# Kernel optimization log

Measured on AMD Instinct MI355X. Metric: run time of the kernel, lower is better.

Reference implementation:

```python
import jax, jax.numpy as jnp
import numpy as np

NUM_HEADS = 6


def setup_inputs() -> dict:
    key = jax.random.key(0)
    k1, k2, k3 = jax.random.split(key, 3)
    b_, n, c = 512, 256, 192
    nw = 64
    x = jax.random.normal(k1, (b_, n, c), dtype=jnp.float32)
    mask = jnp.zeros((nw, n, n), dtype=jnp.float32)  # 0 / -inf additive window mask
    W_qkv = jax.random.normal(k2, (3 * c, c), dtype=jnp.float32) * 0.02
    W_proj = jax.random.normal(k3, (c, c), dtype=jnp.float32) * 0.02
    b_proj = jnp.zeros((c,), dtype=jnp.float32)
    return {"x": x, "mask": mask, "W_qkv": W_qkv, "W_proj": W_proj, "b_proj": b_proj}


def reference(x, mask, W_qkv, W_proj, b_proj):
    b_, n, c = x.shape
    h = NUM_HEADS
    d = c // h
    scale = d ** (-0.5)
    # qkv projection (no bias): (b_, n, 3, h, d) -> (3, b_, h, n, d)
    qkv = (x @ W_qkv.T).reshape(b_, n, 3, h, d).transpose(2, 0, 3, 1, 4)
    q, k, v = qkv[0], qkv[1], qkv[2]
    q = q * scale
    attn = jnp.einsum('bhid,bhjd->bhij', q, k)  # (b_, h, n, n)
    nw = mask.shape[0]
    # add per-window mask bias: view as (B, nw, h, n, n) + (1, nw, 1, n, n)
    attn = attn.reshape(b_ // nw, nw, h, n, n) + mask[None, :, None, :, :]
    attn = attn.reshape(b_, h, n, n)
    attn = jax.nn.softmax(attn, axis=-1)
    out = jnp.einsum('bhij,bhjd->bhid', attn, v)  # (b_, h, n, d)
    out = out.transpose(0, 2, 1, 3).reshape(b_, n, c)
    return out @ W_proj.T + b_proj
```

## Files before the change

kernel.cpp:

```cpp
#include <hip/hip_runtime.h>
#include <hip/hip_bf16.h>
#include <stdint.h>

typedef short bf16x8 __attribute__((ext_vector_type(8)));
typedef float f32x4 __attribute__((ext_vector_type(4)));

#define B_   512
#define N_   256
#define C_   192
#define H_   6
#define D_   32
#define NW_  64

__device__ __forceinline__ uint16_t f2bf(float f) {
    uint32_t u = __builtin_bit_cast(uint32_t, f);
    u += 0x7FFFu + ((u >> 16) & 1u);
    return (uint16_t)(u >> 16);
}

__device__ __forceinline__ uint32_t pk_bf16(float a, float b) {
    float2 t; t.x = a; t.y = b;
    __hip_bfloat162 h = __float22bfloat162_rn(t);
    uint32_t u;
    __builtin_memcpy(&u, &h, 4);
    return u;
}

__device__ __forceinline__ bf16x8 ld_bf8(const uint16_t* p) {
    uint4 u = *reinterpret_cast<const uint4*>(p);
    return __builtin_bit_cast(bf16x8, u);
}

__global__ void prep_kernel(const float* __restrict__ mask,
                            const float* __restrict__ wqkv,
                            const float* __restrict__ wproj,
                            uint16_t* __restrict__ sel,
                            uint16_t* __restrict__ wqkv_bf,
                            uint16_t* __restrict__ wproj_bf,
                            unsigned* __restrict__ flag) {
    const int64_t NSEL = (int64_t)NW_ * N_ * N_;
    const int64_t NWQ  = 3 * C_ * C_;
    const int64_t NWP  = (int64_t)C_ * C_;
    int64_t i = (int64_t)blockIdx.x * blockDim.x + threadIdx.x;
    int64_t stride = (int64_t)gridDim.x * blockDim.x;
    bool nz = false;
    for (; i < NSEL + NWQ + NWP; i += stride) {
        if (i < NSEL) {
            float m = mask[i];
            nz |= (m != 0.0f);
            sel[i] = (m == 0.0f) ? 0xFFFFu : 0u;
        } else if (i < NSEL + NWQ) {
            int64_t j = i - NSEL;
            wqkv_bf[j] = f2bf(wqkv[j]);
        } else {
            int64_t j = i - NSEL - NWQ;
            wproj_bf[j] = f2bf(wproj[j]);
        }
    }
    if (flag && __any(nz) && ((threadIdx.x & 63) == 0))
        atomicOr(flag, 1u);
}

#define SA 200
#define SB 72
__global__ __launch_bounds__(512, 4)
void qkv_kernel(const float* __restrict__ x, const uint16_t* __restrict__ wq,
                uint16_t* __restrict__ qbuf, uint16_t* __restrict__ kbuf,
                uint16_t* __restrict__ vtbuf) {
    __shared__ __align__(16) uint16_t Alds[128 * SA];
    __shared__ __align__(16) uint16_t Blds[192 * SB];
    const int tid  = threadIdx.x;
    const int lane = tid & 63;
    const int wv   = tid >> 6;
    const int wrow = wv >> 2;
    const int wcol = wv & 3;
    const int quad = lane >> 4;
    const int l15  = lane & 15;
    const int m0   = blockIdx.x * 128;

#pragma unroll
    for (int p = 0; p < 12; p++) {
        int f = p * 512 + tid;
        int row = f / 48, c4 = f % 48;
        const float4 v = *reinterpret_cast<const float4*>(
            x + (int64_t)(m0 + row) * 192 + c4 * 4);
        uint2 d;
        d.x = pk_bf16(v.x, v.y);
        d.y = pk_bf16(v.z, v.w);
        *reinterpret_cast<uint2*>(&Alds[row * SA + c4 * 4]) = d;
    }

    const float scale = 0.17677669529663687f * 1.4426950408889634f;

    for (int cb = 0; cb < 3; cb++) {
        f32x4 acc[4][3];
#pragma unroll
        for (int i = 0; i < 4; i++)
#pragma unroll
            for (int j = 0; j < 3; j++) acc[i][j] = (f32x4)0.f;

        for (int k0 = 0; k0 < 192; k0 += 64) {
            uint4 wreg[3];
#pragma unroll
            for (int p = 0; p < 3; p++) {
                int u = p * 512 + tid;
                wreg[p] = *reinterpret_cast<const uint4*>(
                    wq + (int64_t)(cb * 192 + (u >> 3)) * 192 + k0 + (u & 7) * 8);
            }
            __syncthreads();
#pragma unroll
            for (int p = 0; p < 3; p++) {
                int u = p * 512 + tid;
                *reinterpret_cast<uint4*>(&Blds[(u >> 3) * SB + (u & 7) * 8]) = wreg[p];
            }
            __syncthreads();
#pragma unroll
            for (int ks = 0; ks < 2; ks++) {
                bf16x8 xf[4], wf[3];
#pragma unroll
                for (int i = 0; i < 4; i++)
                    xf[i] = *reinterpret_cast<const bf16x8*>(
                        &Alds[(wrow * 64 + i * 16 + l15) * SA + k0 + ks * 32 + quad * 8]);
#pragma unroll
                for (int j = 0; j < 3; j++)
                    wf[j] = *reinterpret_cast<const bf16x8*>(
                        &Blds[(wcol * 48 + j * 16 + l15) * SB + ks * 32 + quad * 8]);
                __builtin_amdgcn_s_setprio(1);
                if (cb < 2) {
#pragma unroll
                    for (int i = 0; i < 4; i++)
#pragma unroll
                        for (int j = 0; j < 3; j++)
                            acc[i][j] = __builtin_amdgcn_mfma_f32_16x16x32_bf16(
                                wf[j], xf[i], acc[i][j], 0, 0, 0);
                } else {
#pragma unroll
                    for (int i = 0; i < 4; i++)
#pragma unroll
                        for (int j = 0; j < 3; j++)
                            acc[i][j] = __builtin_amdgcn_mfma_f32_16x16x32_bf16(
                                xf[i], wf[j], acc[i][j], 0, 0, 0);
                }
                __builtin_amdgcn_s_setprio(0);
            }
        }

        if (cb < 2) {
            uint16_t* dst = (cb == 0) ? qbuf : kbuf;
            const float sc = (cb == 0) ? scale : 1.0f;
#pragma unroll
            for (int i = 0; i < 4; i++) {
                int m = m0 + wrow * 64 + i * 16 + l15;
                int b = m >> 8, pos = m & 255;
#pragma unroll
                for (int j = 0; j < 3; j++) {
                    int cbase = wcol * 48 + j * 16 + quad * 4;
                    int h = cbase >> 5, d0 = cbase & 31;
                    int64_t bh = (int64_t)b * H_ + h;
                    uint2 s;
                    s.x = pk_bf16(acc[i][j][0] * sc, acc[i][j][1] * sc);
                    s.y = pk_bf16(acc[i][j][2] * sc, acc[i][j][3] * sc);
                    *reinterpret_cast<uint2*>(&dst[(bh * N_ + pos) * D_ + d0]) = s;
                }
            }
        } else {
#pragma unroll
            for (int i = 0; i < 4; i++) {
                int m = m0 + wrow * 64 + i * 16 + quad * 4;
                int b = m >> 8, pos0 = m & 255;
#pragma unroll
                for (int j = 0; j < 3; j++) {
                    int c = wcol * 48 + j * 16 + l15;
                    int h = c >> 5, d = c & 31;
                    int64_t bh = (int64_t)b * H_ + h;
                    uint2 s;
                    s.x = pk_bf16(acc[i][j][0], acc[i][j][1]);
                    s.y = pk_bf16(acc[i][j][2], acc[i][j][3]);
                    *reinterpret_cast<uint2*>(&vtbuf[(bh * D_ + d) * N_ + pos0]) = s;
                }
            }
        }
    }
}

__global__ __launch_bounds__(256, 3)
void attn_kernel(const uint16_t* __restrict__ qbuf, const uint16_t* __restrict__ kbuf,
                 const uint16_t* __restrict__ vtbuf, const uint16_t* __restrict__ sel,
                 const unsigned* __restrict__ flag,
                 uint16_t* __restrict__ aout) {
    __shared__ __align__(16) uint16_t Plds[4 * 2 * 32 * 40];
    const int bi = blockIdx.x;
    const int h  = bi % 6;
    const int r_ = bi / 6;
    const int ih = r_ & 1;
    const int g  = (r_ >> 1) & 7;
    const int w  = r_ >> 4;
    const int b  = g * 64 + w;
    const int tid  = threadIdx.x;
    const int lane = tid & 63;
    const int wv   = tid >> 6;
    const int quad = lane >> 4;
    const int l15  = lane & 15;
    const int i0   = ih * 128 + wv * 32;
    const bool hasmask = flag ? (*flag != 0u) : true;
    const int64_t bh = (int64_t)b * H_ + h;
    const uint16_t* qB = qbuf  + bh * N_ * D_;
    const uint16_t* kB = kbuf  + bh * N_ * D_;
    const uint16_t* vB = vtbuf + bh * D_ * N_;
    const uint16_t* sB = sel   + (int64_t)w * N_ * N_;
    uint16_t* Pw = &Plds[wv * 2 * 32 * 40];

    bf16x8 qf[2];
#pragma unroll
    for (int it = 0; it < 2; it++)
        qf[it] = ld_bf8(&qB[(i0 + it * 16 + l15) * D_ + quad * 8]);

    f32x4 oacc[2][2];
    f32x4 lacc[2];
#pragma unroll
    for (int mt = 0; mt < 2; mt++) {
        oacc[mt][0] = (f32x4)0.f; oacc[mt][1] = (f32x4)0.f; lacc[mt] = (f32x4)0.f;
    }
    bf16x8 ones;
#pragma unroll
    for (int e = 0; e < 8; e++) ones[e] = (short)0x3F80;

    bf16x8 kf[4];
#pragma unroll
    for (int jt = 0; jt < 4; jt++)
        kf[jt] = ld_bf8(&kB[(jt * 16 + l15) * D_ + quad * 8]);
    bf16x8 vf[2][2];
#pragma unroll
    for (int hf = 0; hf < 2; hf++)
#pragma unroll
        for (int nt = 0; nt < 2; nt++)
            vf[hf][nt] = ld_bf8(&vB[(nt * 16 + l15) * N_ + hf * 32 + quad * 8]);

    for (int jc = 0; jc < 4; jc++) {
        const int j0 = jc * 64;

        bf16x8 kfn[4], vfn[2][2];
        if (jc < 3) {
#pragma unroll
            for (int jt = 0; jt < 4; jt++)
                kfn[jt] = ld_bf8(&kB[(j0 + 64 + jt * 16 + l15) * D_ + quad * 8]);
#pragma unroll
            for (int hf = 0; hf < 2; hf++)
#pragma unroll
                for (int nt = 0; nt < 2; nt++)
                    vfn[hf][nt] = ld_bf8(&vB[(nt * 16 + l15) * N_ + j0 + 64 + hf * 32 + quad * 8]);
        }

        uint4 sv[2][2];
        if (hasmask) {
#pragma unroll
            for (int hf = 0; hf < 2; hf++)
#pragma unroll
                for (int mt = 0; mt < 2; mt++)
                    sv[hf][mt] = *reinterpret_cast<const uint4*>(
                        &sB[(int64_t)(i0 + mt * 16 + l15) * N_ + j0 + hf * 32 + quad * 8]);
        } else {
#pragma unroll
            for (int hf = 0; hf < 2; hf++)
#pragma unroll
                for (int mt = 0; mt < 2; mt++)
                    sv[hf][mt] = make_uint4(~0u, ~0u, ~0u, ~0u);
        }

#pragma unroll
        for (int hf = 0; hf < 2; hf++) {
            f32x4 sacc[2][2];
#pragma unroll
            for (int jt2 = 0; jt2 < 2; jt2++)
#pragma unroll
                for (int it = 0; it < 2; it++) sacc[jt2][it] = (f32x4)0.f;
            __builtin_amdgcn_s_setprio(1);
#pragma unroll
            for (int jt2 = 0; jt2 < 2; jt2++)
#pragma unroll
                for (int it = 0; it < 2; it++)
                    sacc[jt2][it] = __builtin_amdgcn_mfma_f32_16x16x32_bf16(
                        kf[hf * 2 + jt2], qf[it], sacc[jt2][it], 0, 0, 0);
            __builtin_amdgcn_s_setprio(0);

            uint16_t* Ph = Pw + hf * (32 * 40);
#pragma unroll
            for (int it = 0; it < 2; it++)
#pragma unroll
                for (int jt2 = 0; jt2 < 2; jt2++) {
                    f32x4 s = sacc[jt2][it];
                    uint2 d;
                    d.x = pk_bf16(__builtin_amdgcn_exp2f(s[0]),
                                  __builtin_amdgcn_exp2f(s[1]));
                    d.y = pk_bf16(__builtin_amdgcn_exp2f(s[2]),
                                  __builtin_amdgcn_exp2f(s[3]));
                    *reinterpret_cast<uint2*>(
                        &Ph[(it * 16 + l15) * 40 + jt2 * 16 + quad * 4]) = d;
                }

#pragma unroll
            for (int mt = 0; mt < 2; mt++) {
                uint4 p = *reinterpret_cast<const uint4*>(
                    &Ph[(mt * 16 + l15) * 40 + quad * 8]);
                p.x &= sv[hf][mt].x; p.y &= sv[hf][mt].y;
                p.z &= sv[hf][mt].z; p.w &= sv[hf][mt].w;
                bf16x8 pa = __builtin_bit_cast(bf16x8, p);
                __builtin_amdgcn_s_setprio(1);
                oacc[mt][0] = __builtin_amdgcn_mfma_f32_16x16x32_bf16(pa, vf[hf][0], oacc[mt][0], 0, 0, 0);
                oacc[mt][1] = __builtin_amdgcn_mfma_f32_16x16x32_bf16(pa, vf[hf][1], oacc[mt][1], 0, 0, 0);
                lacc[mt]    = __builtin_amdgcn_mfma_f32_16x16x32_bf16(pa, ones,      lacc[mt],    0, 0, 0);
                __builtin_amdgcn_s_setprio(0);
            }
        }

        if (jc < 3) {
#pragma unroll
            for (int jt = 0; jt < 4; jt++) kf[jt] = kfn[jt];
#pragma unroll
            for (int hf = 0; hf < 2; hf++)
#pragma unroll
                for (int nt = 0; nt < 2; nt++) vf[hf][nt] = vfn[hf][nt];
        }
    }

#pragma unroll
    for (int mt = 0; mt < 2; mt++)
#pragma unroll
        for (int r4 = 0; r4 < 4; r4++) {
            float inv = 1.0f / lacc[mt][r4];
            int i = i0 + mt * 16 + quad * 4 + r4;
#pragma unroll
            for (int nt = 0; nt < 2; nt++) {
                float v = oacc[mt][nt][r4] * inv;
                aout[((int64_t)b * N_ + i) * C_ + h * 32 + nt * 16 + l15] = f2bf(v);
            }
        }
}

__global__ __launch_bounds__(512, 4)
void proj_kernel(const uint16_t* __restrict__ a, const uint16_t* __restrict__ wp,
                 const float* __restrict__ bias, float* __restrict__ out) {
    __shared__ __align__(16) uint16_t Alds[128 * SA];
    const int tid  = threadIdx.x;
    const int lane = tid & 63;
    const int wv   = tid >> 6;
    const int wm   = wv >> 2;
    const int wn   = wv & 3;
    const int quad = lane >> 4;
    const int l15  = lane & 15;
    const int m0   = blockIdx.x * 128;

#pragma unroll
    for (int p = 0; p < 6; p++) {
        int u = p * 512 + tid;
        int row = u / 24, c8 = u % 24;
        uint4 v = *reinterpret_cast<const uint4*>(
            a + (int64_t)(m0 + row) * 192 + c8 * 8);
        *reinterpret_cast<uint4*>(&Alds[row * SA + c8 * 8]) = v;
    }
    __syncthreads();

    f32x4 acc[4][3];
#pragma unroll
    for (int x = 0; x < 4; x++)
#pragma unroll
        for (int y = 0; y < 3; y++) acc[x][y] = (f32x4)0.f;

    const uint16_t* wB = wp + (int64_t)(wn * 48 + l15) * 192;
    bf16x8 bfr[3], bfn[3];
#pragma unroll
    for (int nt = 0; nt < 3; nt++)
        bfr[nt] = ld_bf8(wB + nt * 16 * 192 + quad * 8);

#pragma unroll
    for (int kk = 0; kk < 6; kk++) {
        const int kb = kk * 32;
        if (kk < 5) {
#pragma unroll
            for (int nt = 0; nt < 3; nt++)
                bfn[nt] = ld_bf8(wB + nt * 16 * 192 + kb + 32 + quad * 8);
        }
        bf16x8 af[4];
#pragma unroll
        for (int mt = 0; mt < 4; mt++)
            af[mt] = *reinterpret_cast<const bf16x8*>(
                &Alds[(wm * 64 + mt * 16 + l15) * SA + kb + quad * 8]);
        __builtin_amdgcn_s_setprio(1);
#pragma unroll
        for (int mt = 0; mt < 4; mt++)
#pragma unroll
            for (int nt = 0; nt < 3; nt++)
                acc[mt][nt] = __builtin_amdgcn_mfma_f32_16x16x32_bf16(
                    af[mt], bfr[nt], acc[mt][nt], 0, 0, 0);
        __builtin_amdgcn_s_setprio(0);
        if (kk < 5) {
#pragma unroll
            for (int nt = 0; nt < 3; nt++) bfr[nt] = bfn[nt];
        }
    }

    float bv[3];
#pragma unroll
    for (int nt = 0; nt < 3; nt++) bv[nt] = bias[wn * 48 + nt * 16 + l15];
#pragma unroll
    for (int mt = 0; mt < 4; mt++)
#pragma unroll
        for (int r = 0; r < 4; r++) {
            int m = m0 + wm * 64 + mt * 16 + quad * 4 + r;
#pragma unroll
            for (int nt = 0; nt < 3; nt++) {
                int col = wn * 48 + nt * 16 + l15;
                out[(int64_t)m * 192 + col] = acc[mt][nt][r] + bv[nt];
            }
        }
}

extern "C" void kernel_launch(void* const* d_in, const int* in_sizes, int n_in,
                              void* d_out, int out_size, void* d_ws, size_t ws_size,
                              hipStream_t stream) {
    const float* x     = (const float*)d_in[0];
    const float* mask  = (const float*)d_in[1];
    const float* wqkv  = (const float*)d_in[2];
    const float* wproj = (const float*)d_in[3];
    const float* bproj = (const float*)d_in[4];
    float* out = (float*)d_out;

    uint16_t* qbuf = (uint16_t*)d_out;
    uint16_t* kbuf = qbuf + 25165824;
    char* ws = (char*)d_ws;
    uint16_t* vtbuf = (uint16_t*)(ws);
    uint16_t* aout  = (uint16_t*)(ws + 50331648);
    uint16_t* sel   = (uint16_t*)(ws + 100663296);
    uint16_t* wq_bf = (uint16_t*)(ws + 109051904);
    uint16_t* wp_bf = (uint16_t*)(ws + 109273088);
    unsigned* flag  = nullptr;
    if (ws_size >= 109346816 + 4)
        flag = (unsigned*)(ws + 109346816);

    if (flag) hipMemsetAsync(flag, 0, 4, stream);
    prep_kernel<<<4096, 256, 0, stream>>>(mask, wqkv, wproj, sel, wq_bf, wp_bf, flag);
    qkv_kernel<<<1024, 512, 0, stream>>>(x, wq_bf, qbuf, kbuf, vtbuf);
    attn_kernel<<<6144, 256, 0, stream>>>(qbuf, kbuf, vtbuf, sel, flag, aout);
    proj_kernel<<<1024, 512, 0, stream>>>(aout, wp_bf, bproj, out);
}
```

Before: 379.5 us.

## Vectorize prep kernel, simplify weight staging, drop MFMA priority hints

```diff
diff --git a/kernel.cpp b/kernel.cpp
--- a/kernel.cpp
+++ b/kernel.cpp
@@ -31,30 +31,48 @@
     return __builtin_bit_cast(bf16x8, u);
 }
 
-__global__ void prep_kernel(const float* __restrict__ mask,
-                            const float* __restrict__ wqkv,
-                            const float* __restrict__ wproj,
-                            uint16_t* __restrict__ sel,
-                            uint16_t* __restrict__ wqkv_bf,
-                            uint16_t* __restrict__ wproj_bf,
-                            unsigned* __restrict__ flag) {
-    const int64_t NSEL = (int64_t)NW_ * N_ * N_;
-    const int64_t NWQ  = 3 * C_ * C_;
-    const int64_t NWP  = (int64_t)C_ * C_;
-    int64_t i = (int64_t)blockIdx.x * blockDim.x + threadIdx.x;
-    int64_t stride = (int64_t)gridDim.x * blockDim.x;
+__global__ __launch_bounds__(256)
+void prep_kernel(const float* __restrict__ mask,
+                 const float* __restrict__ wqkv,
+                 const float* __restrict__ wproj,
+                 uint16_t* __restrict__ sel,
+                 uint16_t* __restrict__ wqkv_bf,
+                 uint16_t* __restrict__ wproj_bf,
+                 unsigned* __restrict__ flag) {
+    const int CS = 524288;
+    const int CQ = 13824;
+    const int CP = 4608;
+    int i = blockIdx.x * blockDim.x + threadIdx.x;
+    int stride = gridDim.x * blockDim.x;
     bool nz = false;
-    for (; i < NSEL + NWQ + NWP; i += stride) {
-        if (i < NSEL) {
-            float m = mask[i];
-            nz |= (m != 0.0f);
-            sel[i] = (m == 0.0f) ? 0xFFFFu : 0u;
-        } else if (i < NSEL + NWQ) {
-            int64_t j = i - NSEL;
-            wqkv_bf[j] = f2bf(wqkv[j]);
+    for (int c = i; c < CS + CQ + CP; c += stride) {
+        if (c < CS) {
+            const float4* mp = reinterpret_cast<const float4*>(mask) + (int64_t)c * 2;
+            float4 a = mp[0], b = mp[1];
+            nz |= (a.x != 0.f) | (a.y != 0.f) | (a.z != 0.f) | (a.w != 0.f) |
+                  (b.x != 0.f) | (b.y != 0.f) | (b.z != 0.f) | (b.w != 0.f);
+            uint4 o;
+            o.x = (a.x == 0.f ? 0xFFFFu : 0u) | ((a.y == 0.f ? 0xFFFFu : 0u) << 16);
+            o.y = (a.z == 0.f ? 0xFFFFu : 0u) | ((a.w == 0.f ? 0xFFFFu : 0u) << 16);
+            o.z = (b.x == 0.f ? 0xFFFFu : 0u) | ((b.y == 0.f ? 0xFFFFu : 0u) << 16);
+            o.w = (b.z == 0.f ? 0xFFFFu : 0u) | ((b.w == 0.f ? 0xFFFFu : 0u) << 16);
+            *reinterpret_cast<uint4*>(sel + (int64_t)c * 8) = o;
+        } else if (c < CS + CQ) {
+            int j = c - CS;
+            const float4* wp4 = reinterpret_cast<const float4*>(wqkv) + (int64_t)j * 2;
+            float4 a = wp4[0], b = wp4[1];
+            uint4 o;
+            o.x = pk_bf16(a.x, a.y); o.y = pk_bf16(a.z, a.w);
+            o.z = pk_bf16(b.x, b.y); o.w = pk_bf16(b.z, b.w);
+            *reinterpret_cast<uint4*>(wqkv_bf + (int64_t)j * 8) = o;
         } else {
-            int64_t j = i - NSEL - NWQ;
-            wproj_bf[j] = f2bf(wproj[j]);
+            int j = c - CS - CQ;
+            const float4* wp4 = reinterpret_cast<const float4*>(wproj) + (int64_t)j * 2;
+            float4 a = wp4[0], b = wp4[1];
+            uint4 o;
+            o.x = pk_bf16(a.x, a.y); o.y = pk_bf16(a.z, a.w);
+            o.z = pk_bf16(b.x, b.y); o.w = pk_bf16(b.z, b.w);
+            *reinterpret_cast<uint4*>(wproj_bf + (int64_t)j * 8) = o;
         }
     }
     if (flag && __any(nz) && ((threadIdx.x & 63) == 0))
@@ -100,18 +118,14 @@
             for (int j = 0; j < 3; j++) acc[i][j] = (f32x4)0.f;
 
         for (int k0 = 0; k0 < 192; k0 += 64) {
-            uint4 wreg[3];
+            __syncthreads();
 #pragma unroll
             for (int p = 0; p < 3; p++) {
                 int u = p * 512 + tid;
-                wreg[p] = *reinterpret_cast<const uint4*>(
-                    wq + (int64_t)(cb * 192 + (u >> 3)) * 192 + k0 + (u & 7) * 8);
-            }
-            __syncthreads();
-#pragma unroll
-            for (int p = 0; p < 3; p++) {
-                int u = p * 512 + tid;
-                *reinterpret_cast<uint4*>(&Blds[(u >> 3) * SB + (u & 7) * 8]) = wreg[p];
+                int row = u >> 3, c8 = u & 7;
+                uint4 w = *reinterpret_cast<const uint4*>(
+                    wq + (int64_t)(cb * 192 + row) * 192 + k0 + c8 * 8);
+                *reinterpret_cast<uint4*>(&Blds[row * SB + c8 * 8]) = w;
             }
             __syncthreads();
 #pragma unroll
@@ -125,7 +139,6 @@
                 for (int j = 0; j < 3; j++)
                     wf[j] = *reinterpret_cast<const bf16x8*>(
                         &Blds[(wcol * 48 + j * 16 + l15) * SB + ks * 32 + quad * 8]);
-                __builtin_amdgcn_s_setprio(1);
                 if (cb < 2) {
 #pragma unroll
                     for (int i = 0; i < 4; i++)
@@ -141,7 +154,6 @@
                             acc[i][j] = __builtin_amdgcn_mfma_f32_16x16x32_bf16(
                                 xf[i], wf[j], acc[i][j], 0, 0, 0);
                 }
-                __builtin_amdgcn_s_setprio(0);
             }
         }
 
@@ -385,14 +397,12 @@
         for (int mt = 0; mt < 4; mt++)
             af[mt] = *reinterpret_cast<const bf16x8*>(
                 &Alds[(wm * 64 + mt * 16 + l15) * SA + kb + quad * 8]);
-        __builtin_amdgcn_s_setprio(1);
 #pragma unroll
         for (int mt = 0; mt < 4; mt++)
 #pragma unroll
             for (int nt = 0; nt < 3; nt++)
                 acc[mt][nt] = __builtin_amdgcn_mfma_f32_16x16x32_bf16(
                     af[mt], bfr[nt], acc[mt][nt], 0, 0, 0);
-        __builtin_amdgcn_s_setprio(0);
         if (kk < 5) {
 #pragma unroll
             for (int nt = 0; nt < 3; nt++) bfr[nt] = bfn[nt];
@@ -438,7 +448,7 @@
         flag = (unsigned*)(ws + 109346816);
 
     if (flag) hipMemsetAsync(flag, 0, 4, stream);
-    prep_kernel<<<4096, 256, 0, stream>>>(mask, wqkv, wproj, sel, wq_bf, wp_bf, flag);
+    prep_kernel<<<2048, 256, 0, stream>>>(mask, wqkv, wproj, sel, wq_bf, wp_bf, flag);
     qkv_kernel<<<1024, 512, 0, stream>>>(x, wq_bf, qbuf, kbuf, vtbuf);
     attn_kernel<<<6144, 256, 0, stream>>>(qbuf, kbuf, vtbuf, sel, flag, aout);
     proj_kernel<<<1024, 512, 0, stream>>>(aout, wp_bf, bproj, out);
```

Measured after the change: 330.4 us. 1.15x faster.
